# Kernel tuning notes

Hardware: AMD Instinct MI355X
Metric: run time of the kernel (lower is better)

The kernel has to match this reference:

```python
import jax, jax.numpy as jnp
import numpy as np

N_NODES = 200000
N_EDGES = 6400000
D_FEAT = 128
N_CLASSES = 40


def setup_inputs() -> dict:
    key = jax.random.key(0)
    ks = jax.random.split(key, 10)
    s_in = 1.0 / np.sqrt(D_FEAT)
    return {
        "x": jax.random.normal(ks[0], (N_NODES, D_FEAT), dtype=jnp.float32),
        "edge_index": jax.random.randint(ks[1], (2, N_EDGES), 0, N_NODES, dtype=jnp.int64),
        "W0": jax.random.normal(ks[2], (D_FEAT, D_FEAT), dtype=jnp.float32) * s_in,
        "b0": jnp.zeros((D_FEAT,), dtype=jnp.float32),
        "W1": jax.random.normal(ks[3], (D_FEAT, D_FEAT), dtype=jnp.float32) * s_in,
        "b1": jnp.zeros((D_FEAT,), dtype=jnp.float32),
        "W2": jax.random.normal(ks[4], (D_FEAT, D_FEAT), dtype=jnp.float32) * s_in,
        "b2": jnp.zeros((D_FEAT,), dtype=jnp.float32),
        "W3": jax.random.normal(ks[5], (D_FEAT, N_CLASSES), dtype=jnp.float32) * s_in,
        "b3": jnp.zeros((N_CLASSES,), dtype=jnp.float32),
    }


def _silu(h):
    return h * jax.nn.sigmoid(h)


def reference(x, edge_index, W0, b0, W1, b1, W2, b2, W3, b3):
    # PyG ChebConv with K=1: out = Tx_0 @ weight[0] + bias, Tx_0 = x.
    # edge_index feeds the scaled-Laplacian norm, which is unused when K == 1.
    del edge_index
    h = _silu(x @ W0 + b0)            # [N, D] ChebConv + SiLU
    h = _silu(h @ W1 + b1)            # [N, D]
    h = _silu(h @ W2 + b2)            # [N, D]
    logits = h @ W3 + b3              # [N, C]
    return jax.nn.log_softmax(logits, axis=1)
```

## Files before the change

### kernel.cpp

```cpp
#include <hip/hip_runtime.h>

#define NN 200000

typedef __attribute__((ext_vector_type(8))) short bf16x8;
typedef __attribute__((ext_vector_type(4))) float f32x4;
typedef __attribute__((ext_vector_type(4))) unsigned int u32x4;

static __device__ __forceinline__ short f2bf(float f) {
    unsigned u = __builtin_bit_cast(unsigned, f);
    u += 0x7fffu + ((u >> 16) & 1u);
    return (short)(u >> 16);
}

static __device__ __forceinline__ int swz(int r, int k) {
    return (r << 7) + (((k >> 3) ^ (r & 15)) << 3) + (k & 7);
}

__global__ void prep_weights_k(const float* __restrict__ W0, const float* __restrict__ W1,
                               const float* __restrict__ W2, const float* __restrict__ W3,
                               short* __restrict__ wt) {
    int e = blockIdx.x * 256 + threadIdx.x;
    if (e < 49152) {
        int l = e >> 14;
        int i = e & 16383;
        int n = i >> 7, k = i & 127;
        const float* W = (l == 0) ? W0 : ((l == 1) ? W1 : W2);
        wt[e] = f2bf(W[(k << 7) + n]);
    } else if (e < 55296) {
        int i = e - 49152;
        int n = i >> 7, k = i & 127;
        wt[e] = (n < 40) ? f2bf(W3[k * 40 + n]) : (short)0;
    }
}

__global__ __launch_bounds__(256, 2)
void mlp_fused_k(const float* __restrict__ x, const short* __restrict__ wt,
                 const float* __restrict__ b0, const float* __restrict__ b1,
                 const float* __restrict__ b2, const float* __restrict__ b3,
                 float* __restrict__ out) {
    __shared__ __align__(16) short sA[128 * 128];
    __shared__ __align__(16) short sW[128 * 128];

    const int tid  = (int)threadIdx.x;
    const int lane = tid & 63;
    const int wv   = tid >> 6;
    const int m    = lane & 15;
    const int quad = lane >> 4;
    const int rb   = (int)blockIdx.x * 128;
    const int rwb  = wv * 32;

    auto stageW = [&](int chunk_base, int nchunks) {
        const u32x4* src = (const u32x4*)wt + chunk_base;
        #pragma unroll
        for (int i = 0; i < 8; ++i) {
            int q = tid + (i << 8);
            if (q < nchunks) {
                int r = q >> 4, c = q & 15;
                *(u32x4*)&sW[(r << 7) + ((c ^ (r & 15)) << 3)] = src[q];
            }
        }
    };

    f32x4 acc[2][8];
    auto zacc = [&]() {
        #pragma unroll
        for (int rt = 0; rt < 2; ++rt)
            #pragma unroll
            for (int ct = 0; ct < 8; ++ct)
                #pragma unroll
                for (int r = 0; r < 4; ++r) acc[rt][ct][r] = 0.f;
    };

    auto computeA = [&]() {
        zacc();
        #pragma unroll
        for (int ks = 0; ks < 4; ++ks) {
            int kk = (ks << 5) + (quad << 3);
            bf16x8 a0 = *(const bf16x8*)&sA[swz(rwb + m, kk)];
            bf16x8 a1 = *(const bf16x8*)&sA[swz(rwb + 16 + m, kk)];
            #pragma unroll
            for (int ct = 0; ct < 8; ++ct) {
                bf16x8 b = *(const bf16x8*)&sW[swz((ct << 4) + m, kk)];
                acc[0][ct] = __builtin_amdgcn_mfma_f32_16x16x32_bf16(a0, b, acc[0][ct], 0, 0, 0);
                acc[1][ct] = __builtin_amdgcn_mfma_f32_16x16x32_bf16(a1, b, acc[1][ct], 0, 0, 0);
            }
        }
    };

    auto epilogue = [&](const float* __restrict__ bias) {
        float bv[8];
        #pragma unroll
        for (int ct = 0; ct < 8; ++ct) bv[ct] = bias[(ct << 4) + m];
        #pragma unroll
        for (int rt = 0; rt < 2; ++rt)
            #pragma unroll
            for (int ct = 0; ct < 8; ++ct)
                #pragma unroll
                for (int r = 0; r < 4; ++r) {
                    float v = acc[rt][ct][r] + bv[ct];
                    float h = v * __builtin_amdgcn_rcpf(1.f + __expf(-v));
                    int rl = rwb + (rt << 4) + (quad << 2) + r;
                    sA[swz(rl, (ct << 4) + m)] = f2bf(h);
                }
    };

    stageW(0, 2048);
    __syncthreads();
    zacc();
    {
        int g0 = rb + rwb + m, g1 = g0 + 16;
        int row0 = (g0 < NN) ? g0 : (NN - 1);
        int row1 = (g1 < NN) ? g1 : (NN - 1);
        const float* p0 = x + ((long)row0 << 7) + (quad << 3);
        const float* p1 = x + ((long)row1 << 7) + (quad << 3);
        #pragma unroll
        for (int ks = 0; ks < 4; ++ks) {
            f32x4 v0a = *(const f32x4*)(p0 + (ks << 5));
            f32x4 v0b = *(const f32x4*)(p0 + (ks << 5) + 4);
            f32x4 v1a = *(const f32x4*)(p1 + (ks << 5));
            f32x4 v1b = *(const f32x4*)(p1 + (ks << 5) + 4);
            bf16x8 a0, a1;
            #pragma unroll
            for (int j = 0; j < 4; ++j) {
                a0[j] = f2bf(v0a[j]); a0[j + 4] = f2bf(v0b[j]);
                a1[j] = f2bf(v1a[j]); a1[j + 4] = f2bf(v1b[j]);
            }
            int kk = (ks << 5) + (quad << 3);
            #pragma unroll
            for (int ct = 0; ct < 8; ++ct) {
                bf16x8 b = *(const bf16x8*)&sW[swz((ct << 4) + m, kk)];
                acc[0][ct] = __builtin_amdgcn_mfma_f32_16x16x32_bf16(a0, b, acc[0][ct], 0, 0, 0);
                acc[1][ct] = __builtin_amdgcn_mfma_f32_16x16x32_bf16(a1, b, acc[1][ct], 0, 0, 0);
            }
        }
    }
    __syncthreads();
    epilogue(b0);
    stageW(2048, 2048);
    __syncthreads();

    computeA();
    __syncthreads();
    epilogue(b1);
    stageW(4096, 2048);
    __syncthreads();

    computeA();
    __syncthreads();
    epilogue(b2);
    stageW(6144, 768);
    __syncthreads();

    f32x4 c3[2][3];
    #pragma unroll
    for (int rt = 0; rt < 2; ++rt)
        #pragma unroll
        for (int ct = 0; ct < 3; ++ct)
            #pragma unroll
            for (int r = 0; r < 4; ++r) c3[rt][ct][r] = 0.f;
    #pragma unroll
    for (int ks = 0; ks < 4; ++ks) {
        int kk = (ks << 5) + (quad << 3);
        bf16x8 a0 = *(const bf16x8*)&sA[swz(rwb + m, kk)];
        bf16x8 a1 = *(const bf16x8*)&sA[swz(rwb + 16 + m, kk)];
        #pragma unroll
        for (int ct = 0; ct < 3; ++ct) {
            bf16x8 b = *(const bf16x8*)&sW[swz((ct << 4) + m, kk)];
            c3[0][ct] = __builtin_amdgcn_mfma_f32_16x16x32_bf16(a0, b, c3[0][ct], 0, 0, 0);
            c3[1][ct] = __builtin_amdgcn_mfma_f32_16x16x32_bf16(a1, b, c3[1][ct], 0, 0, 0);
        }
    }
    const bool val2 = (m < 8);
    float bv0 = b3[m];
    float bv1 = b3[16 + m];
    float bv2 = val2 ? b3[32 + m] : 0.f;
    #pragma unroll
    for (int rt = 0; rt < 2; ++rt) {
        #pragma unroll
        for (int r = 0; r < 4; ++r) {
            float v0 = c3[rt][0][r] + bv0;
            float v1 = c3[rt][1][r] + bv1;
            float v2 = c3[rt][2][r] + bv2;
            float mx = fmaxf(v0, v1);
            mx = val2 ? fmaxf(mx, v2) : mx;
            #pragma unroll
            for (int s = 1; s < 16; s <<= 1)
                mx = fmaxf(mx, __shfl_xor(mx, s, 64));
            float sm = __expf(v0 - mx) + __expf(v1 - mx) + (val2 ? __expf(v2 - mx) : 0.f);
            #pragma unroll
            for (int s = 1; s < 16; s <<= 1)
                sm += __shfl_xor(sm, s, 64);
            float L = mx + __logf(sm);
            int grow = rb + rwb + (rt << 4) + (quad << 2) + r;
            if (grow < NN) {
                float* orow = out + (long)grow * 40;
                orow[m]      = v0 - L;
                orow[16 + m] = v1 - L;
                if (val2) orow[32 + m] = v2 - L;
            }
        }
    }
}

extern "C" void kernel_launch(void* const* d_in, const int* in_sizes, int n_in,
                              void* d_out, int out_size, void* d_ws, size_t ws_size,
                              hipStream_t stream) {
    const float* x   = (const float*)d_in[0];
    const float* W0  = (const float*)d_in[2];
    const float* bb0 = (const float*)d_in[3];
    const float* W1  = (const float*)d_in[4];
    const float* bb1 = (const float*)d_in[5];
    const float* W2  = (const float*)d_in[6];
    const float* bb2 = (const float*)d_in[7];
    const float* W3  = (const float*)d_in[8];
    const float* bb3 = (const float*)d_in[9];
    short* wt  = (short*)d_ws;
    float* out = (float*)d_out;

    hipLaunchKernelGGL(prep_weights_k, dim3(216), dim3(256), 0, stream, W0, W1, W2, W3, wt);
    hipLaunchKernelGGL(mlp_fused_k, dim3((NN + 127) / 128), dim3(256), 0, stream,
                       x, wt, bb0, bb1, bb2, bb3, out);
}
```

Baseline: 265.0 us.

## Read weights directly from global/L2 and drop LDS weight staging and block syncs

Removes the shared-memory weight tiles and all __syncthreads; each wave now keeps its own 32-row activation tile in LDS and reads the bf16 weight fragments straight from global memory, which should hit in cache because the weights are small. This halves LDS use so launch bounds rise to 4 blocks per CU for more occupancy. It also adds a cheaper packed bf16 conversion (round-half-up via perm) and nontemporal loads of x and stores of the output. The cost is repeated global/L2 weight traffic per wave and a slightly different rounding mode.

After: 341.7 us. 28.9% more time.

```diff
diff --git a/kernel.cpp b/kernel.cpp
--- a/kernel.cpp
+++ b/kernel.cpp
@@ -10,6 +10,12 @@
     unsigned u = __builtin_bit_cast(unsigned, f);
     u += 0x7fffu + ((u >> 16) & 1u);
     return (short)(u >> 16);
+}
+
+static __device__ __forceinline__ unsigned pk2(float a, float b) {
+    unsigned ua = __builtin_bit_cast(unsigned, a) + 0x8000u;
+    unsigned ub = __builtin_bit_cast(unsigned, b) + 0x8000u;
+    return __builtin_amdgcn_perm(ub, ua, 0x07060302u);
 }
 
 static __device__ __forceinline__ int swz(int r, int k) {
@@ -33,33 +39,22 @@
     }
 }
 
-__global__ __launch_bounds__(256, 2)
+__global__ __launch_bounds__(256, 4)
 void mlp_fused_k(const float* __restrict__ x, const short* __restrict__ wt,
                  const float* __restrict__ b0, const float* __restrict__ b1,
                  const float* __restrict__ b2, const float* __restrict__ b3,
                  float* __restrict__ out) {
-    __shared__ __align__(16) short sA[128 * 128];
-    __shared__ __align__(16) short sW[128 * 128];
+    __shared__ __align__(16) short sA[4][32 * 128];
 
     const int tid  = (int)threadIdx.x;
     const int lane = tid & 63;
     const int wv   = tid >> 6;
     const int m    = lane & 15;
     const int quad = lane >> 4;
-    const int rb   = (int)blockIdx.x * 128;
-    const int rwb  = wv * 32;
-
-    auto stageW = [&](int chunk_base, int nchunks) {
-        const u32x4* src = (const u32x4*)wt + chunk_base;
-        #pragma unroll
-        for (int i = 0; i < 8; ++i) {
-            int q = tid + (i << 8);
-            if (q < nchunks) {
-                int r = q >> 4, c = q & 15;
-                *(u32x4*)&sW[(r << 7) + ((c ^ (r & 15)) << 3)] = src[q];
-            }
-        }
-    };
+    short* sAw = &sA[wv][0];
+    const int grow0 = (int)blockIdx.x * 128 + wv * 32;
+
+    const short* wb = wt + m * 128 + quad * 8;
 
     f32x4 acc[2][8];
     auto zacc = [&]() {
@@ -69,22 +64,6 @@
             for (int ct = 0; ct < 8; ++ct)
                 #pragma unroll
                 for (int r = 0; r < 4; ++r) acc[rt][ct][r] = 0.f;
-    };
-
-    auto computeA = [&]() {
-        zacc();
-        #pragma unroll
-        for (int ks = 0; ks < 4; ++ks) {
-            int kk = (ks << 5) + (quad << 3);
-            bf16x8 a0 = *(const bf16x8*)&sA[swz(rwb + m, kk)];
-            bf16x8 a1 = *(const bf16x8*)&sA[swz(rwb + 16 + m, kk)];
-            #pragma unroll
-            for (int ct = 0; ct < 8; ++ct) {
-                bf16x8 b = *(const bf16x8*)&sW[swz((ct << 4) + m, kk)];
-                acc[0][ct] = __builtin_amdgcn_mfma_f32_16x16x32_bf16(a0, b, acc[0][ct], 0, 0, 0);
-                acc[1][ct] = __builtin_amdgcn_mfma_f32_16x16x32_bf16(a1, b, acc[1][ct], 0, 0, 0);
-            }
-        }
     };
 
     auto epilogue = [&](const float* __restrict__ bias) {
@@ -99,57 +78,64 @@
                 for (int r = 0; r < 4; ++r) {
                     float v = acc[rt][ct][r] + bv[ct];
                     float h = v * __builtin_amdgcn_rcpf(1.f + __expf(-v));
-                    int rl = rwb + (rt << 4) + (quad << 2) + r;
-                    sA[swz(rl, (ct << 4) + m)] = f2bf(h);
+                    int rl = (rt << 4) + (quad << 2) + r;
+                    unsigned u = __builtin_bit_cast(unsigned, h) + 0x8000u;
+                    sAw[swz(rl, (ct << 4) + m)] = (short)(u >> 16);
                 }
     };
 
-    stageW(0, 2048);
-    __syncthreads();
-    zacc();
-    {
-        int g0 = rb + rwb + m, g1 = g0 + 16;
-        int row0 = (g0 < NN) ? g0 : (NN - 1);
-        int row1 = (g1 < NN) ? g1 : (NN - 1);
-        const float* p0 = x + ((long)row0 << 7) + (quad << 3);
-        const float* p1 = x + ((long)row1 << 7) + (quad << 3);
+    auto dense = [&](int lbase) {
+        zacc();
         #pragma unroll
         for (int ks = 0; ks < 4; ++ks) {
-            f32x4 v0a = *(const f32x4*)(p0 + (ks << 5));
-            f32x4 v0b = *(const f32x4*)(p0 + (ks << 5) + 4);
-            f32x4 v1a = *(const f32x4*)(p1 + (ks << 5));
-            f32x4 v1b = *(const f32x4*)(p1 + (ks << 5) + 4);
-            bf16x8 a0, a1;
-            #pragma unroll
-            for (int j = 0; j < 4; ++j) {
-                a0[j] = f2bf(v0a[j]); a0[j + 4] = f2bf(v0b[j]);
-                a1[j] = f2bf(v1a[j]); a1[j + 4] = f2bf(v1b[j]);
-            }
             int kk = (ks << 5) + (quad << 3);
+            bf16x8 a0 = *(const bf16x8*)&sAw[swz(m, kk)];
+            bf16x8 a1 = *(const bf16x8*)&sAw[swz(16 + m, kk)];
+            const short* wk = wb + lbase + (ks << 5);
             #pragma unroll
             for (int ct = 0; ct < 8; ++ct) {
-                bf16x8 b = *(const bf16x8*)&sW[swz((ct << 4) + m, kk)];
+                bf16x8 b = *(const bf16x8*)(wk + (ct << 11));
                 acc[0][ct] = __builtin_amdgcn_mfma_f32_16x16x32_bf16(a0, b, acc[0][ct], 0, 0, 0);
                 acc[1][ct] = __builtin_amdgcn_mfma_f32_16x16x32_bf16(a1, b, acc[1][ct], 0, 0, 0);
             }
         }
-    }
-    __syncthreads();
+    };
+
+    zacc();
+    {
+        int g0 = grow0 + m, g1 = g0 + 16;
+        long r0 = (g0 < NN) ? g0 : (NN - 1);
+        long r1 = (g1 < NN) ? g1 : (NN - 1);
+        const f32x4* p0 = (const f32x4*)(x + (r0 << 7)) + quad * 2;
+        const f32x4* p1 = (const f32x4*)(x + (r1 << 7)) + quad * 2;
+        #pragma unroll
+        for (int ks = 0; ks < 4; ++ks) {
+            f32x4 v0a = __builtin_nontemporal_load(p0 + ks * 8);
+            f32x4 v0b = __builtin_nontemporal_load(p0 + ks * 8 + 1);
+            f32x4 v1a = __builtin_nontemporal_load(p1 + ks * 8);
+            f32x4 v1b = __builtin_nontemporal_load(p1 + ks * 8 + 1);
+            u32x4 ua0, ua1;
+            ua0[0] = pk2(v0a[0], v0a[1]); ua0[1] = pk2(v0a[2], v0a[3]);
+            ua0[2] = pk2(v0b[0], v0b[1]); ua0[3] = pk2(v0b[2], v0b[3]);
+            ua1[0] = pk2(v1a[0], v1a[1]); ua1[1] = pk2(v1a[2], v1a[3]);
+            ua1[2] = pk2(v1b[0], v1b[1]); ua1[3] = pk2(v1b[2], v1b[3]);
+            bf16x8 a0 = __builtin_bit_cast(bf16x8, ua0);
+            bf16x8 a1 = __builtin_bit_cast(bf16x8, ua1);
+            const short* wk = wb + (ks << 5);
+            #pragma unroll
+            for (int ct = 0; ct < 8; ++ct) {
+                bf16x8 b = *(const bf16x8*)(wk + (ct << 11));
+                acc[0][ct] = __builtin_amdgcn_mfma_f32_16x16x32_bf16(a0, b, acc[0][ct], 0, 0, 0);
+                acc[1][ct] = __builtin_amdgcn_mfma_f32_16x16x32_bf16(a1, b, acc[1][ct], 0, 0, 0);
+            }
+        }
+    }
     epilogue(b0);
-    stageW(2048, 2048);
-    __syncthreads();
-
-    computeA();
-    __syncthreads();
+
+    dense(16384);
     epilogue(b1);
-    stageW(4096, 2048);
-    __syncthreads();
-
-    computeA();
-    __syncthreads();
+    dense(32768);
     epilogue(b2);
-    stageW(6144, 768);
-    __syncthreads();
 
     f32x4 c3[2][3];
     #pragma unroll
@@ -161,11 +147,12 @@
     #pragma unroll
     for (int ks = 0; ks < 4; ++ks) {
         int kk = (ks << 5) + (quad << 3);
-        bf16x8 a0 = *(const bf16x8*)&sA[swz(rwb + m, kk)];
-        bf16x8 a1 = *(const bf16x8*)&sA[swz(rwb + 16 + m, kk)];
+        bf16x8 a0 = *(const bf16x8*)&sAw[swz(m, kk)];
+        bf16x8 a1 = *(const bf16x8*)&sAw[swz(16 + m, kk)];
+        const short* wk = wb + 49152 + (ks << 5);
         #pragma unroll
         for (int ct = 0; ct < 3; ++ct) {
-            bf16x8 b = *(const bf16x8*)&sW[swz((ct << 4) + m, kk)];
+            bf16x8 b = *(const bf16x8*)(wk + (ct << 11));
             c3[0][ct] = __builtin_amdgcn_mfma_f32_16x16x32_bf16(a0, b, c3[0][ct], 0, 0, 0);
             c3[1][ct] = __builtin_amdgcn_mfma_f32_16x16x32_bf16(a1, b, c3[1][ct], 0, 0, 0);
         }
@@ -191,12 +178,12 @@
             for (int s = 1; s < 16; s <<= 1)
                 sm += __shfl_xor(sm, s, 64);
             float L = mx + __logf(sm);
-            int grow = rb + rwb + (rt << 4) + (quad << 2) + r;
+            int grow = grow0 + (rt << 4) + (quad << 2) + r;
             if (grow < NN) {
                 float* orow = out + (long)grow * 40;
-                orow[m]      = v0 - L;
-                orow[16 + m] = v1 - L;
-                if (val2) orow[32 + m] = v2 - L;
+                __builtin_nontemporal_store(v0 - L, orow + m);
+                __builtin_nontemporal_store(v1 - L, orow + 16 + m);
+                if (val2) __builtin_nontemporal_store(v2 - L, orow + 32 + m);
             }
         }
     }
```
